# Kernel optimization log

Hardware: AMD Instinct MI355X
Metric: run time of the kernel (lower is better)

## Reference

```python
import jax, jax.numpy as jnp
import numpy as np

B, S, D, H = 2, 2048, 1024, 16
HD = D // H
SPARSITY = 0.1
LAMBDA_MAX = 10.0
ALPHA = 5.0


def local_prior_mask(seq_len: int, sparsity: float) -> jnp.ndarray:
    # |i - j| <= window_size // 2, window_size = int(seq_len * sparsity)
    window_size = max(1, int(seq_len * sparsity))
    rows = jnp.arange(seq_len)[:, None]
    cols = jnp.arange(seq_len)[None, :]
    return jnp.abs(rows - cols) <= (window_size // 2)


def setup_inputs() -> dict:
    key = jax.random.key(0)
    ks = jax.random.split(key, 12)
    scale = 1.0 / np.sqrt(D)
    inp = {
        'x': jax.random.normal(ks[0], (B, S, D), dtype=jnp.float32),
        'u_prev': jax.random.uniform(ks[1], (B, 1), dtype=jnp.float32),
        'Wq': jax.random.normal(ks[2], (D, D), dtype=jnp.float32) * scale,
        'bq': jnp.zeros((D,), dtype=jnp.float32),
        'Wk': jax.random.normal(ks[3], (D, D), dtype=jnp.float32) * scale,
        'bk': jnp.zeros((D,), dtype=jnp.float32),
        'Wv': jax.random.normal(ks[4], (D, D), dtype=jnp.float32) * scale,
        'bv': jnp.zeros((D,), dtype=jnp.float32),
        'Wo': jax.random.normal(ks[5], (D, D), dtype=jnp.float32) * scale,
        'bo': jnp.zeros((D,), dtype=jnp.float32),
    }
    return inp


def reference(x, u_prev, Wq, bq, Wk, bk, Wv, bv, Wo, bo):
    b, s, _ = x.shape
    # projections (torch Linear: y = x W^T + b)
    def proj(W, bias):
        return (x @ W.T + bias).reshape(b, s, H, HD).transpose(0, 2, 1, 3)  # [B,H,S,HD]
    q = proj(Wq, bq)
    k = proj(Wk, bk)
    v = proj(Wv, bv)

    # dynamic gating: lambda = lambda_max * exp(-alpha * u_prev), shape [B,1,1,1]
    lam = (LAMBDA_MAX * jnp.exp(-ALPHA * u_prev)).reshape(b, 1, 1, 1)

    prior = local_prior_mask(s, SPARSITY)  # [S,S] bool

    scores = jnp.einsum('bhqd,bhkd->bhqk', q, k) / jnp.sqrt(jnp.asarray(HD, x.dtype))
    # additive prior bias: penalize positions outside the structural prior by -lambda
    scores = scores - lam * (~prior).astype(x.dtype)

    attn = jax.nn.softmax(scores, axis=-1)
    out = jnp.einsum('bhqk,bhkd->bhqd', attn, v)           # [B,H,S,HD]
    out = out.transpose(0, 2, 1, 3).reshape(b, s, D)        # [B,S,D]
    out = out @ Wo.T + bo
    return out, lam.reshape(b, 1)
```

## Files before the change

kernel.cpp:

```cpp
#include <hip/hip_runtime.h>

typedef __attribute__((ext_vector_type(8))) short short8;
typedef __attribute__((ext_vector_type(4))) float f32x4;

#define MFMA16(a,b,c) __builtin_amdgcn_mfma_f32_16x16x32_bf16(a,b,c,0,0,0)

__device__ __forceinline__ unsigned short f2bf(float f){
  unsigned int u = __float_as_uint(f);
  u += 0x7FFF + ((u>>16)&1);
  return (unsigned short)(u>>16);
}

__device__ __forceinline__ float fexp2(float x){
#if __has_builtin(__builtin_amdgcn_exp2f)
  return __builtin_amdgcn_exp2f(x);
#else
  return exp2f(x);
#endif
}

__device__ __forceinline__ void gl_lds16(const void* g, void* l){
  __builtin_amdgcn_global_load_lds((const __attribute__((address_space(1))) void*)g,
                                   (__attribute__((address_space(3))) void*)l, 16, 0, 0);
}

__global__ void cvt_bf16(const float* __restrict__ src, unsigned short* __restrict__ dst, int n){
  int i = (blockIdx.x*blockDim.x + threadIdx.x)*4;
  if (i + 3 < n){
    float4 v = *(const float4*)(src + i);
    ushort4 o;
    o.x = f2bf(v.x); o.y = f2bf(v.y); o.z = f2bf(v.z); o.w = f2bf(v.w);
    *(ushort4*)(dst + i) = o;
  }
}

template<int MODE>
__global__ __launch_bounds__(256) void gemm_bt(
  const unsigned short* __restrict__ A,
  const unsigned short* __restrict__ Bw,
  const float* __restrict__ bias0, const float* __restrict__ bias1, const float* __restrict__ bias2,
  unsigned short* __restrict__ Qo, unsigned short* __restrict__ Ko, unsigned short* __restrict__ VTo,
  float* __restrict__ Co,
  int M, int N, int K)
{
  __shared__ unsigned short As[2][128*32];
  __shared__ unsigned short Bs[2][128*32];
  const int tid = threadIdx.x;
  const int m0 = blockIdx.y*128, n0 = blockIdx.x*128;
  const int w = tid>>6, lane = tid&63, lr = lane&15, lg = lane>>4;
  const int wm = w>>1, wn = w&1;
  const int nk = K/32;

  auto stage = [&](int buf, int kt){
    const unsigned short* Ag = A + (size_t)m0*K + kt*32;
    const unsigned short* Bg = Bw + (size_t)n0*K + kt*32;
    #pragma unroll
    for (int it=0; it<2; ++it){
      int slot = it*256 + tid;
      gl_lds16(Ag + (size_t)(slot>>2)*K + (slot&3)*8, &As[buf][slot*8]);
    }
    #pragma unroll
    for (int it=0; it<2; ++it){
      int slot = it*256 + tid;
      gl_lds16(Bg + (size_t)(slot>>2)*K + (slot&3)*8, &Bs[buf][slot*8]);
    }
  };

  f32x4 acc[4][4] = {};
  stage(0,0);
  for (int kt=0; kt<nk; ++kt){
    int cur = kt&1;
    __syncthreads();
    if (kt+1 < nk) stage(cur^1, kt+1);
    short8 af[4], bfr[4];
    #pragma unroll
    for (int i=0;i<4;++i) af[i]  = *(const short8*)&As[cur][(wm*64 + i*16 + lr)*32 + lg*8];
    #pragma unroll
    for (int j=0;j<4;++j) bfr[j] = *(const short8*)&Bs[cur][(wn*64 + j*16 + lr)*32 + lg*8];
    #pragma unroll
    for (int i=0;i<4;++i)
      #pragma unroll
      for (int j=0;j<4;++j)
        acc[i][j] = MFMA16(af[i], bfr[j], acc[i][j]);
  }

  #pragma unroll
  for (int i=0;i<4;++i){
    #pragma unroll
    for (int j=0;j<4;++j){
      const int n  = n0 + wn*64 + j*16 + lr;
      const int mb = m0 + wm*64 + i*16 + lg*4;
      if (MODE==0){
        const int which = n>>10, nn = n&1023;
        const float bv = (which==0) ? bias0[nn] : (which==1) ? bias1[nn] : bias2[nn];
        const int h = nn>>6, hd = nn&63;
        #pragma unroll
        for (int r=0;r<4;++r){
          const int m = mb + r;
          const int b = m>>11, s = m&2047;
          const unsigned short u = f2bf(acc[i][j][r] + bv);
          const size_t bh = (size_t)(b*16 + h);
          if (which==0)      Qo[(bh*2048 + s)*64 + hd] = u;
          else if (which==1) Ko[(bh*2048 + s)*64 + hd] = u;
          else               VTo[(bh*64 + hd)*2048 + s] = u;
        }
      } else {
        const float bv = bias0[n];
        #pragma unroll
        for (int r=0;r<4;++r){
          const int m = mb + r;
          Co[(size_t)m*N + n] = acc[i][j][r] + bv;
        }
      }
    }
  }
}

__global__ __launch_bounds__(256, 4) void attn_k(
  const unsigned short* __restrict__ Qb,
  const unsigned short* __restrict__ Kb,
  const unsigned short* __restrict__ VT,
  const float* __restrict__ u_prev,
  unsigned short* __restrict__ Out)
{
  const int qt = blockIdx.x, bh = blockIdx.y;
  const int b = bh>>4, h = bh&15;
  const float lam = 10.f * __expf(-5.f * u_prev[b]);
  const float nlamb = -lam * 1.4426950408889634f;
  const int tid = threadIdx.x;
  const int w = tid>>6, lane = tid&63, lr = lane&15, lg = lane>>4;
  const int q0 = qt*64 + w*16;

  const unsigned short* Qp = Qb + (size_t)bh*2048*64;
  const unsigned short* Kp = Kb + (size_t)bh*2048*64;
  const unsigned short* Vp = VT + (size_t)bh*64*2048;

  __shared__ unsigned short Ks[2][2048];
  __shared__ unsigned short Vs[2][2048];
  __shared__ unsigned short p_lds[4][16][40];

  const unsigned short* ksrc = Kp + (tid&31)*64 + (tid>>5)*8;
  const unsigned short* vsrc = Vp + (size_t)(tid&63)*2048 + (tid>>6)*8;
  unsigned short* kd0 = &Ks[0][tid*8];
  unsigned short* kd1 = &Ks[1][tid*8];
  unsigned short* vd0 = &Vs[0][tid*8];
  unsigned short* vd1 = &Vs[1][tid*8];

  const unsigned short* kf0p = &Ks[0][(lg*32+lr)*8];
  const unsigned short* kf1p = &Ks[1][(lg*32+lr)*8];
  const unsigned short* vf0p = &Vs[0][(lg*64+lr)*8];
  const unsigned short* vf1p = &Vs[1][(lg*64+lr)*8];
  const unsigned short* pap  = &p_lds[w][lr][lg*8];
  unsigned short* pwp = &p_lds[w][lg*4][lr];

  short8 qf0 = *(const short8*)&Qp[(size_t)(q0+lr)*64 +      lg*8];
  short8 qf1 = *(const short8*)&Qp[(size_t)(q0+lr)*64 + 32 + lg*8];

  const float c1 = 0.18033688011112042f;
  float l_run[4] = {0.f, 0.f, 0.f, 0.f};
  f32x4 o0 = {}, o1 = {}, o2 = {}, o3 = {};
  const f32x4 zf = {};
  f32x4 s0, s1, t0, t1;

#define STAGE_(KD, VD, KT) do{ const int kw_ = (KT)&63; \
    gl_lds16(ksrc + ((size_t)kw_<<11), (KD)); \
    gl_lds16(vsrc + (kw_<<5), (VD)); }while(0)

#define QKM_(KP, S0, S1) do{ \
    short8 ka_ = *(const short8*)(KP); \
    short8 kb_ = *(const short8*)((KP)+1024); \
    short8 kc_ = *(const short8*)((KP)+128); \
    short8 kd_ = *(const short8*)((KP)+1152); \
    S0 = MFMA16(qf0, ka_, zf); S0 = MFMA16(qf1, kb_, S0); \
    S1 = MFMA16(qf0, kc_, zf); S1 = MFMA16(qf1, kd_, S1); }while(0)

#define BODY_(KT, VFPC, KDC, VDC, KFPN, SIN0, SIN1, SOUT0, SOUT1) do{ \
    const int k0_ = (KT)*32; \
    const int cls_ = (k0_ > q0 + 117 || k0_ < q0 - 133) ? 2 \
                   : (k0_ >= q0 - 87 && k0_ <= q0 + 71) ? 0 : 1; \
    _Pragma("unroll") \
    for (int r=0;r<4;++r){ \
      const int qi_ = q0 + lg*4 + r; \
      float b0 = 0.f, b1 = 0.f; \
      if (cls_ == 2){ b0 = nlamb; b1 = nlamb; } \
      else if (cls_ == 1){ \
        int d0 = qi_ - (k0_ + lr);      if (d0<0) d0 = -d0; \
        int d1 = qi_ - (k0_ + 16 + lr); if (d1<0) d1 = -d1; \
        if (d0 > 102) b0 = nlamb; \
        if (d1 > 102) b1 = nlamb; \
      } \
      const float p0 = fexp2(fmaf((SIN0)[r], c1, b0)); \
      const float p1 = fexp2(fmaf((SIN1)[r], c1, b1)); \
      l_run[r] += p0 + p1; \
      pwp[r*40]      = (unsigned short)(__float_as_uint(p0)>>16); \
      pwp[r*40 + 16] = (unsigned short)(__float_as_uint(p1)>>16); \
    } \
    short8 vfa_ = *(const short8*)(VFPC); \
    short8 vfb_ = *(const short8*)((VFPC)+128); \
    short8 vfc_ = *(const short8*)((VFPC)+256); \
    short8 vfd_ = *(const short8*)((VFPC)+384); \
    short8 pa_  = *(const short8*)(pap); \
    __syncthreads(); \
    STAGE_((KDC), (VDC), (KT)+2); \
    QKM_((KFPN), SOUT0, SOUT1); \
    o0 = MFMA16(pa_, vfa_, o0); \
    o1 = MFMA16(pa_, vfb_, o1); \
    o2 = MFMA16(pa_, vfc_, o2); \
    o3 = MFMA16(pa_, vfd_, o3); }while(0)

  STAGE_(kd0, vd0, 0);
  __syncthreads();
  STAGE_(kd1, vd1, 1);
  QKM_(kf0p, s0, s1);

  for (int kt2=0; kt2<32; ++kt2){
    BODY_(2*kt2,   vf0p, kd0, vd0, kf1p, s0, s1, t0, t1);
    BODY_(2*kt2+1, vf1p, kd1, vd1, kf0p, t0, t1, s0, s1);
  }
#undef BODY_
#undef QKM_
#undef STAGE_

  #pragma unroll
  for (int off=1; off<16; off<<=1)
    #pragma unroll
    for (int r=0;r<4;++r)
      l_run[r] += __shfl_xor(l_run[r], off, 64);

  #pragma unroll
  for (int r=0;r<4;++r){
    const int qi = q0 + lg*4 + r;
    const float linv = 1.0f / l_run[r];
    unsigned short* op = &Out[((size_t)b*2048 + qi)*1024 + h*64 + lr];
    op[0]  = f2bf(o0[r] * linv);
    op[16] = f2bf(o1[r] * linv);
    op[32] = f2bf(o2[r] * linv);
    op[48] = f2bf(o3[r] * linv);
  }
}

__global__ void tail_k(const float* __restrict__ u, float* __restrict__ out){
  int i = threadIdx.x;
  if (i < 2) out[4194304 + i] = 10.f*__expf(-5.f*u[i]);
}

extern "C" void kernel_launch(void* const* d_in, const int* in_sizes, int n_in,
                              void* d_out, int out_size, void* d_ws, size_t ws_size,
                              hipStream_t stream){
  const float* x  = (const float*)d_in[0];
  const float* u  = (const float*)d_in[1];
  const float* Wq = (const float*)d_in[2];
  const float* bq = (const float*)d_in[3];
  const float* Wk = (const float*)d_in[4];
  const float* bk = (const float*)d_in[5];
  const float* Wv = (const float*)d_in[6];
  const float* bv = (const float*)d_in[7];
  const float* Wo = (const float*)d_in[8];
  const float* bo = (const float*)d_in[9];
  float* out = (float*)d_out;

  unsigned char* ws = (unsigned char*)d_ws;
  unsigned short* xb    = (unsigned short*)(ws);
  unsigned short* attnb = xb;
  unsigned short* Wqkvb = (unsigned short*)(ws + 8388608);
  unsigned short* Wob   = (unsigned short*)(ws + 14680064);
  unsigned short* Qb2   = (unsigned short*)(ws + 16777216);
  unsigned short* Kb2   = (unsigned short*)(ws + 25165824);
  unsigned short* VTb   = (unsigned short*)(ws + 33554432);

  cvt_bf16<<<4096, 256, 0, stream>>>(x,  xb, 4194304);
  cvt_bf16<<<1024, 256, 0, stream>>>(Wq, Wqkvb,            1048576);
  cvt_bf16<<<1024, 256, 0, stream>>>(Wk, Wqkvb + 1048576,  1048576);
  cvt_bf16<<<1024, 256, 0, stream>>>(Wv, Wqkvb + 2097152,  1048576);
  cvt_bf16<<<1024, 256, 0, stream>>>(Wo, Wob, 1048576);

  gemm_bt<0><<<dim3(24,32), 256, 0, stream>>>(xb, Wqkvb, bq, bk, bv,
                                              Qb2, Kb2, VTb, nullptr, 4096, 3072, 1024);
  attn_k<<<dim3(32,32), 256, 0, stream>>>(Qb2, Kb2, VTb, u, attnb);
  gemm_bt<1><<<dim3(8,32), 256, 0, stream>>>(attnb, Wob, bo, nullptr, nullptr,
                                             nullptr, nullptr, nullptr, out, 4096, 1024, 1024);
  tail_k<<<1, 64, 0, stream>>>(u, out);
}
```

Baseline: 154.3 us.

## Triple-buffer K/V tiles with partial vmcnt waits in attention loop

Moves the K/V LDS staging from double to triple buffering, so each iteration prefetches tile kt+3. The full __syncthreads is replaced by an inline s_waitcnt vmcnt(2) plus s_barrier, which lets the newest global-to-LDS loads stay in flight across the barrier. The loop is unrolled by three with a peeled final tile. This hides more global load latency at the cost of extra LDS per block, which may lower occupancy, and it depends on hand-counted waitcnt values being correct.

New measurement: 153.8 us. About the same (-0.3%).

```diff
diff --git a/kernel.cpp b/kernel.cpp
--- a/kernel.cpp
+++ b/kernel.cpp
@@ -135,21 +135,25 @@
   const unsigned short* Kp = Kb + (size_t)bh*2048*64;
   const unsigned short* Vp = VT + (size_t)bh*64*2048;
 
-  __shared__ unsigned short Ks[2][2048];
-  __shared__ unsigned short Vs[2][2048];
+  __shared__ unsigned short Ks[3][2048];
+  __shared__ unsigned short Vs[3][2048];
   __shared__ unsigned short p_lds[4][16][40];
 
   const unsigned short* ksrc = Kp + (tid&31)*64 + (tid>>5)*8;
   const unsigned short* vsrc = Vp + (size_t)(tid&63)*2048 + (tid>>6)*8;
   unsigned short* kd0 = &Ks[0][tid*8];
   unsigned short* kd1 = &Ks[1][tid*8];
+  unsigned short* kd2 = &Ks[2][tid*8];
   unsigned short* vd0 = &Vs[0][tid*8];
   unsigned short* vd1 = &Vs[1][tid*8];
+  unsigned short* vd2 = &Vs[2][tid*8];
 
   const unsigned short* kf0p = &Ks[0][(lg*32+lr)*8];
   const unsigned short* kf1p = &Ks[1][(lg*32+lr)*8];
+  const unsigned short* kf2p = &Ks[2][(lg*32+lr)*8];
   const unsigned short* vf0p = &Vs[0][(lg*64+lr)*8];
   const unsigned short* vf1p = &Vs[1][(lg*64+lr)*8];
+  const unsigned short* vf2p = &Vs[2][(lg*64+lr)*8];
   const unsigned short* pap  = &p_lds[w][lr][lg*8];
   unsigned short* pwp = &p_lds[w][lg*4][lr];
 
@@ -160,11 +164,15 @@
   float l_run[4] = {0.f, 0.f, 0.f, 0.f};
   f32x4 o0 = {}, o1 = {}, o2 = {}, o3 = {};
   const f32x4 zf = {};
-  f32x4 s0, s1, t0, t1;
+  f32x4 sA0, sA1, sB0, sB1, sC0, sC1;
 
 #define STAGE_(KD, VD, KT) do{ const int kw_ = (KT)&63; \
     gl_lds16(ksrc + ((size_t)kw_<<11), (KD)); \
     gl_lds16(vsrc + (kw_<<5), (VD)); }while(0)
+
+#define BAR_ do{ \
+    asm volatile("s_waitcnt vmcnt(2) lgkmcnt(0)\n\ts_barrier" ::: "memory"); \
+    __builtin_amdgcn_sched_barrier(0); }while(0)
 
 #define QKM_(KP, S0, S1) do{ \
     short8 ka_ = *(const short8*)(KP); \
@@ -174,7 +182,7 @@
     S0 = MFMA16(qf0, ka_, zf); S0 = MFMA16(qf1, kb_, S0); \
     S1 = MFMA16(qf0, kc_, zf); S1 = MFMA16(qf1, kd_, S1); }while(0)
 
-#define BODY_(KT, VFPC, KDC, VDC, KFPN, SIN0, SIN1, SOUT0, SOUT1) do{ \
+#define SOFT_(KT, SIN0, SIN1) do{ \
     const int k0_ = (KT)*32; \
     const int cls_ = (k0_ > q0 + 117 || k0_ < q0 - 133) ? 2 \
                    : (k0_ >= q0 - 87 && k0_ <= q0 + 71) ? 0 : 1; \
@@ -194,14 +202,17 @@
       l_run[r] += p0 + p1; \
       pwp[r*40]      = (unsigned short)(__float_as_uint(p0)>>16); \
       pwp[r*40 + 16] = (unsigned short)(__float_as_uint(p1)>>16); \
-    } \
+    } }while(0)
+
+#define BODY_(KT, VFPC, KDC, VDC, KFPN, SIN0, SIN1, SOUT0, SOUT1) do{ \
+    SOFT_((KT), SIN0, SIN1); \
     short8 vfa_ = *(const short8*)(VFPC); \
     short8 vfb_ = *(const short8*)((VFPC)+128); \
     short8 vfc_ = *(const short8*)((VFPC)+256); \
     short8 vfd_ = *(const short8*)((VFPC)+384); \
     short8 pa_  = *(const short8*)(pap); \
-    __syncthreads(); \
-    STAGE_((KDC), (VDC), (KT)+2); \
+    BAR_; \
+    STAGE_((KDC), (VDC), (KT)+3); \
     QKM_((KFPN), SOUT0, SOUT1); \
     o0 = MFMA16(pa_, vfa_, o0); \
     o1 = MFMA16(pa_, vfb_, o1); \
@@ -209,16 +220,35 @@
     o3 = MFMA16(pa_, vfd_, o3); }while(0)
 
   STAGE_(kd0, vd0, 0);
-  __syncthreads();
   STAGE_(kd1, vd1, 1);
-  QKM_(kf0p, s0, s1);
-
-  for (int kt2=0; kt2<32; ++kt2){
-    BODY_(2*kt2,   vf0p, kd0, vd0, kf1p, s0, s1, t0, t1);
-    BODY_(2*kt2+1, vf1p, kd1, vd1, kf0p, t0, t1, s0, s1);
+  STAGE_(kd2, vd2, 2);
+  BAR_;
+  QKM_(kf0p, sA0, sA1);
+
+  for (int it=0; it<21; ++it){
+    const int kt = it*3;
+    BODY_(kt,   vf0p, kd0, vd0, kf1p, sA0, sA1, sB0, sB1);
+    BODY_(kt+1, vf1p, kd1, vd1, kf2p, sB0, sB1, sC0, sC1);
+    BODY_(kt+2, vf2p, kd2, vd2, kf0p, sC0, sC1, sA0, sA1);
+  }
+  {
+    SOFT_(63, sA0, sA1);
+    short8 vfa_ = *(const short8*)(vf0p);
+    short8 vfb_ = *(const short8*)(vf0p+128);
+    short8 vfc_ = *(const short8*)(vf0p+256);
+    short8 vfd_ = *(const short8*)(vf0p+384);
+    asm volatile("s_waitcnt lgkmcnt(0)" ::: "memory");
+    __builtin_amdgcn_sched_barrier(0);
+    short8 pa_  = *(const short8*)(pap);
+    o0 = MFMA16(pa_, vfa_, o0);
+    o1 = MFMA16(pa_, vfb_, o1);
+    o2 = MFMA16(pa_, vfc_, o2);
+    o3 = MFMA16(pa_, vfd_, o3);
   }
 #undef BODY_
+#undef SOFT_
 #undef QKM_
+#undef BAR_
 #undef STAGE_
 
   #pragma unroll
```
